# Kernel optimization log

Measured on AMD Instinct MI355X. Metric: run time of the kernel, lower is better.

## Reference

```python
import jax, jax.numpy as jnp
import numpy as np

# Planck radiance in wavenumber form: B(nu, T) = c1*nu^3 / (exp(c2*nu/T) - 1)
# nu in cm^-1, T in Kelvin, B in W / (m^2 sr cm^-1)
C1 = 1.191042e-8
C2 = 1.4387752
N_TEMPS = 20


def planck_radiance(nu, T):
    return C1 * nu ** 3 / jnp.expm1(C2 * nu / T)


def setup_inputs() -> dict:
    key = jax.random.key(0)
    k1, k2, k3 = jax.random.split(key, 3)
    N, C = 1048576, 54  # 1024x1024 pixels, 54 spectral channels
    wg = jnp.linspace(720.0, 1250.0, C, dtype=jnp.float32)
    v = (wg - wg.min()) / (wg.max() - wg.min())
    pi = 3.14159
    library = jnp.stack([
        jnp.full((C,), 0.98),                      # skin
        0.9 + 0.05 * jnp.sin(2 * pi * v),          # fabric_cotton
        0.15 + 0.1 * v,                            # metal_aluminum
        0.95 - 0.03 * v,                           # vegetation
        0.92 + 0.02 * jnp.sin(4 * pi * v),         # concrete
        0.85 + 0.1 * v,                            # glass
    ]).astype(jnp.float32)
    # realistic LWIR radiance magnitudes (~0.02-0.12 W/m^2/sr/cm^-1)
    s_sky = 0.05 * jax.random.uniform(k1, (C,), dtype=jnp.float32)
    s_ground = 0.08 + 0.02 * jax.random.uniform(k2, (C,), dtype=jnp.float32)
    s_obs = 0.02 + 0.1 * jax.random.uniform(k3, (N, C), dtype=jnp.float32)
    return {"s_obs": s_obs, "s_sky": s_sky, "s_ground": s_ground,
            "library": library, "wavenumber_grid": wg}


def reference(s_obs, s_sky, s_ground, library, wavenumber_grid):
    N, C = s_obs.shape
    M = library.shape[0]
    t_cand = jnp.linspace(250.0, 350.0, N_TEMPS, dtype=s_obs.dtype)
    # All candidate model spectra are pixel-independent (V fixed at 0.5):
    x_amb = 0.5 * s_sky + 0.5 * s_ground                           # [C]
    B = planck_radiance(wavenumber_grid[None, :], t_cand[:, None])  # [T, C]
    s_model = library[:, None, :] * B[None, :, :] \
        + (1.0 - library[:, None, :]) * x_amb                       # [M, T, C]
    cand = s_model.reshape(M * N_TEMPS, C)  # row-major: idx = m*T + t, matches loop order
    # ||s_obs - cand||^2 expanded: memory-bound [N, M*T] loss matrix
    losses = (jnp.sum(s_obs ** 2, axis=-1, keepdims=True)
              - 2.0 * s_obs @ cand.T
              + jnp.sum(cand ** 2, axis=-1))                        # [N, M*T]
    best = jnp.argmin(losses, axis=-1)                              # first-min, matches strict '<'
    best_loss = jnp.take_along_axis(losses, best[:, None], axis=1)[:, 0]
    m_idx = best // N_TEMPS
    t_idx = best % N_TEMPS
    best_t = t_cand[t_idx]                                          # [N]
    best_e = library[m_idx]                                         # [N, C]
    best_v = jnp.full((N,), 0.5, dtype=s_obs.dtype)
    s_recon = best_e * planck_radiance(wavenumber_grid[None, :], best_t[:, None]) \
        + (1.0 - best_e) * x_amb                                    # [N, C]
    texture = best_e.mean(axis=-1)
    beta = jnp.zeros((N, 1), dtype=s_obs.dtype)
    objective = best_loss.mean()
    return (best_t, best_e, best_v, beta, texture, s_recon, objective)
```

## Files before the change

### kernel.cpp

```cpp
#include <hip/hip_runtime.h>
#include <math.h>

#define C_CH 54
#define CP   64
#define NT   20
#define NM   6
#define NK   120
#define BLK  256
#define PIX_PER_BLK BLK
#define NF4  (NK * CP / 4)

typedef float f4 __attribute__((ext_vector_type(4)));

__global__ __launch_bounds__(256) void hadar_prep(
    const float* __restrict__ s_sky, const float* __restrict__ s_ground,
    const float* __restrict__ library, const float* __restrict__ wg,
    float* __restrict__ cand)
{
    __shared__ float xamb[C_CH];
    __shared__ float tc[NT];
    __shared__ float lm[NM];
    const int tid = threadIdx.x;
    if (tid < NT) tc[tid] = 250.0f + (float)tid * (100.0f / 19.0f);
    if (tid < C_CH) xamb[tid] = 0.5f * s_sky[tid] + 0.5f * s_ground[tid];
    if (tid < NM) {
        float s = 0.0f;
        for (int c = 0; c < C_CH; ++c) s += library[tid * C_CH + c];
        lm[tid] = s / (float)C_CH;
    }
    __syncthreads();

    const float c1 = 1.191042e-8f, c2 = 1.4387752f;
    for (int idx = tid; idx < NK * CP; idx += 256) {
        const int k = idx >> 6, c = idx & 63;
        float v = 0.0f;
        if (c < C_CH) {
            const int m = k / NT, t = k - m * NT;
            const float nu = wg[c];
            const float B = c1 * nu * nu * nu / expm1f(c2 * nu / tc[t]);
            const float e = library[m * C_CH + c];
            v = e * B + (1.0f - e) * xamb[c];
        }
        cand[idx] = v;
    }
    __syncthreads();

    if (tid < NK) {
        float s = 0.0f;
        for (int c = 0; c < C_CH; ++c) { float v = cand[tid * CP + c]; s += v * v; }
        const int m = tid / NT, t = tid - m * NT;
        cand[tid * CP + 54] = s;
        cand[tid * CP + 55] = tc[t];
        cand[tid * CP + 56] = lm[m];
    }
}


#define LOADH(B, F4OFF) { \
    const f4* __restrict__ Lr = Lc + (F4OFF); \
    _Pragma("unroll") for (int j = 0; j < 7; ++j) B[j] = Lr[j]; }

#define FMAPH(B, CB) { \
    _Pragma("unroll") for (int j = 0; j < 7; ++j) { \
        _Pragma("unroll") for (int e = 0; e < 4; ++e) { \
            const int c = (CB) + 4 * j + e; \
            if (c < C_CH) a[c & 3] += row0[c] * B[j][e]; \
        } } }

__global__ __launch_bounds__(BLK)
__attribute__((amdgpu_waves_per_eu(2, 2)))
void hadar_main(
    const float* __restrict__ s_obs,
    const float* __restrict__ library,
    const float* __restrict__ cand,
    float* __restrict__ out, float* __restrict__ partials, int N)
{
    __shared__ f4 ldsc[NF4];
    __shared__ int2 bkm[PIX_PER_BLK];
    __shared__ float red[BLK];

    const int tid = threadIdx.x;
    const long long base = (long long)blockIdx.x * PIX_PER_BLK;
    const long long n0 = base + tid;
    const bool v0 = (n0 < N);

    float row0[C_CH];
    if (v0) {
        const float2* rp = (const float2*)(s_obs + n0 * C_CH);
        #pragma unroll
        for (int i = 0; i < C_CH / 2; ++i) {
            float2 w = rp[i];
            row0[2 * i] = w.x; row0[2 * i + 1] = w.y;
        }
    } else {
        #pragma unroll
        for (int c = 0; c < C_CH; ++c) row0[c] = 0.0f;
    }

    {
        const f4* __restrict__ gc = (const f4*)cand;
        for (int j = tid; j < NF4; j += BLK) ldsc[j] = gc[j];
    }

    float ssq0 = 0.0f;
    #pragma unroll
    for (int c = 0; c < C_CH; ++c) ssq0 += row0[c] * row0[c];

    float bl0 = 3.4e38f;
    int bk0 = NK;

    __syncthreads();

    const f4* __restrict__ Lc = ldsc;

    f4 P[7], Q[7];
    int f0 = 0;
    LOADH(P, 0);
    #pragma unroll 1
    for (int k = 0; k < NK; ++k) {
        LOADH(Q, f0 + 7);
        float a[4] = {0.f, 0.f, 0.f, 0.f};
        FMAPH(P, 0);
        const int fn = (k + 1 < NK) ? f0 + 16 : 0;
        LOADH(P, fn);
        FMAPH(Q, 28);
        const float sq = Q[6][2];
        const float d = (a[0] + a[1]) + (a[2] + a[3]);
        const float l = (ssq0 - 2.0f * d) + sq;
        if (l < bl0) { bl0 = l; bk0 = k; }
        f0 = fn;
    }

    if (!v0 || bk0 >= NK) bk0 = 0;

    const size_t NN = (size_t)N;
    const size_t NC = (size_t)C_CH * NN;
    const float* __restrict__ Lf = (const float*)ldsc;

    if (v0) {
        out[n0] = Lf[bk0 * CP + 55];
        out[NN + NC + n0] = 0.5f;
        out[2 * NN + NC + n0] = 0.0f;
        out[3 * NN + NC + n0] = Lf[bk0 * CP + 56];
    }

    bkm[tid] = make_int2(bk0 * CP, (bk0 / NT) * C_CH);

    float lsum = v0 ? bl0 : 0.0f;
    __syncthreads();

    {
        float* __restrict__ be = out + NN + (size_t)base * C_CH;
        float* __restrict__ sr = out + 4 * NN + NC + (size_t)base * C_CH;
        int p = tid / C_CH;
        int c = tid - p * C_CH;
        #pragma unroll 2
        for (int j = tid; j < PIX_PER_BLK * C_CH; j += BLK) {
            const int2 o = bkm[p];
            const float ev = library[o.y + c];
            const float sv = Lf[o.x + c];
            if (base + p < N) { be[j] = ev; sr[j] = sv; }
            p += 4; c += 40;
            if (c >= C_CH) { c -= C_CH; ++p; }
        }
    }

    red[tid] = lsum;
    __syncthreads();
    #pragma unroll
    for (int s = BLK / 2; s > 0; s >>= 1) {
        if (tid < s) red[tid] += red[tid + s];
        __syncthreads();
    }
    if (tid == 0) partials[blockIdx.x] = red[0];
}

__global__ __launch_bounds__(256) void hadar_reduce(
    const float* __restrict__ partials, int nb, float* __restrict__ obj_out, float invN)
{
    __shared__ float red[256];
    float s = 0.0f;
    for (int i = threadIdx.x; i < nb; i += 256) s += partials[i];
    red[threadIdx.x] = s;
    __syncthreads();
    #pragma unroll
    for (int st = 128; st > 0; st >>= 1) {
        if (threadIdx.x < st) red[threadIdx.x] += red[threadIdx.x + st];
        __syncthreads();
    }
    if (threadIdx.x == 0) *obj_out = red[0] * invN;
}

extern "C" void kernel_launch(void* const* d_in, const int* in_sizes, int n_in,
                              void* d_out, int out_size, void* d_ws, size_t ws_size,
                              hipStream_t stream)
{
    const float* s_obs    = (const float*)d_in[0];
    const float* s_sky    = (const float*)d_in[1];
    const float* s_ground = (const float*)d_in[2];
    const float* library  = (const float*)d_in[3];
    const float* wg       = (const float*)d_in[4];
    float* out = (float*)d_out;

    const int N  = in_sizes[0] / C_CH;
    const int nb = (N + PIX_PER_BLK - 1) / PIX_PER_BLK;

    float* ws       = (float*)d_ws;
    float* cand     = ws;
    float* partials = ws + 8192;

    hadar_prep<<<1, 256, 0, stream>>>(s_sky, s_ground, library, wg, cand);
    hadar_main<<<nb, BLK, 0, stream>>>(s_obs, library, cand, out, partials, N);

    const size_t NN = (size_t)N;
    float* obj_out = out + 4 * NN + 2 * (size_t)C_CH * NN;
    hadar_reduce<<<1, 256, 0, stream>>>(partials, nb, obj_out, 1.0f / (float)N);
}
```

Baseline: 889.8 us.

## Read candidate spectra through scalar loads instead of LDS in main loop

The candidate table is no longer staged in shared memory. Each iteration of the 120-candidate loop now fetches one candidate row into scalar registers with s_load_dwordx16/x8 inline asm, and the FMA loop uses those scalar operands directly. This removes the LDS fill, a barrier, and the per-thread LDS reads, which frees LDS and drops the fixed waves-per-EU limit. In exchange, every iteration serialises on an lgkmcnt(0) wait with no prefetch overlap, and the gather stage now reads from global memory rather than LDS.

After: 732.8 us. 1.21x faster.

```diff
diff --git a/kernel.cpp b/kernel.cpp
--- a/kernel.cpp
+++ b/kernel.cpp
@@ -8,9 +8,9 @@
 #define NK   120
 #define BLK  256
 #define PIX_PER_BLK BLK
-#define NF4  (NK * CP / 4)
 
-typedef float f4 __attribute__((ext_vector_type(4)));
+typedef float sf16 __attribute__((ext_vector_type(16)));
+typedef float sf8  __attribute__((ext_vector_type(8)));
 
 __global__ __launch_bounds__(256) void hadar_prep(
     const float* __restrict__ s_sky, const float* __restrict__ s_ground,
@@ -55,30 +55,14 @@
     }
 }
 
+#define CE(c) ((c) < 16 ? q0[(c)] : (c) < 32 ? q1[(c)-16] : (c) < 48 ? q2[(c)-32] : q3[(c)-48])
 
-#define LOADH(B, F4OFF) { \
-    const f4* __restrict__ Lr = Lc + (F4OFF); \
-    _Pragma("unroll") for (int j = 0; j < 7; ++j) B[j] = Lr[j]; }
-
-#define FMAPH(B, CB) { \
-    _Pragma("unroll") for (int j = 0; j < 7; ++j) { \
-        _Pragma("unroll") for (int e = 0; e < 4; ++e) { \
-            const int c = (CB) + 4 * j + e; \
-            if (c < C_CH) a[c & 3] += row0[c] * B[j][e]; \
-        } } }
-
-__global__ __launch_bounds__(BLK)
-__attribute__((amdgpu_waves_per_eu(2, 2)))
-void hadar_main(
+__global__ __launch_bounds__(BLK) void hadar_main(
     const float* __restrict__ s_obs,
     const float* __restrict__ library,
     const float* __restrict__ cand,
     float* __restrict__ out, float* __restrict__ partials, int N)
 {
-    __shared__ f4 ldsc[NF4];
-    __shared__ int2 bkm[PIX_PER_BLK];
-    __shared__ float red[BLK];
-
     const int tid = threadIdx.x;
     const long long base = (long long)blockIdx.x * PIX_PER_BLK;
     const long long n0 = base + tid;
@@ -97,53 +81,49 @@
         for (int c = 0; c < C_CH; ++c) row0[c] = 0.0f;
     }
 
-    {
-        const f4* __restrict__ gc = (const f4*)cand;
-        for (int j = tid; j < NF4; j += BLK) ldsc[j] = gc[j];
-    }
-
     float ssq0 = 0.0f;
     #pragma unroll
     for (int c = 0; c < C_CH; ++c) ssq0 += row0[c] * row0[c];
 
     float bl0 = 3.4e38f;
-    int bk0 = NK;
+    int bk0 = 0;
 
-    __syncthreads();
-
-    const f4* __restrict__ Lc = ldsc;
-
-    f4 P[7], Q[7];
-    int f0 = 0;
-    LOADH(P, 0);
+    const float* pk = cand;
     #pragma unroll 1
     for (int k = 0; k < NK; ++k) {
-        LOADH(Q, f0 + 7);
+        sf16 q0, q1, q2;
+        sf8  q3;
+        asm volatile("s_load_dwordx16 %0, %1, 0x0"  : "=s"(q0) : "s"(pk));
+        asm volatile("s_load_dwordx16 %0, %1, 0x40" : "=s"(q1) : "s"(pk));
+        asm volatile("s_load_dwordx16 %0, %1, 0x80" : "=s"(q2) : "s"(pk));
+        asm volatile("s_load_dwordx8  %0, %1, 0xc0" : "=s"(q3) : "s"(pk));
+        asm volatile("s_waitcnt lgkmcnt(0)" : "+s"(q0), "+s"(q1), "+s"(q2), "+s"(q3));
+
         float a[4] = {0.f, 0.f, 0.f, 0.f};
-        FMAPH(P, 0);
-        const int fn = (k + 1 < NK) ? f0 + 16 : 0;
-        LOADH(P, fn);
-        FMAPH(Q, 28);
-        const float sq = Q[6][2];
+        #pragma unroll
+        for (int c = 0; c < C_CH; ++c) {
+            a[c & 3] += row0[c] * CE(c);
+        }
+        const float sq = q3[6];
         const float d = (a[0] + a[1]) + (a[2] + a[3]);
         const float l = (ssq0 - 2.0f * d) + sq;
         if (l < bl0) { bl0 = l; bk0 = k; }
-        f0 = fn;
+
+        pk += CP;
     }
-
-    if (!v0 || bk0 >= NK) bk0 = 0;
 
     const size_t NN = (size_t)N;
     const size_t NC = (size_t)C_CH * NN;
-    const float* __restrict__ Lf = (const float*)ldsc;
 
     if (v0) {
-        out[n0] = Lf[bk0 * CP + 55];
+        const float* cr = cand + (size_t)bk0 * CP;
+        out[n0] = cr[55];
         out[NN + NC + n0] = 0.5f;
         out[2 * NN + NC + n0] = 0.0f;
-        out[3 * NN + NC + n0] = Lf[bk0 * CP + 56];
+        out[3 * NN + NC + n0] = cr[56];
     }
 
+    __shared__ int2 bkm[PIX_PER_BLK];
     bkm[tid] = make_int2(bk0 * CP, (bk0 / NT) * C_CH);
 
     float lsum = v0 ? bl0 : 0.0f;
@@ -158,13 +138,14 @@
         for (int j = tid; j < PIX_PER_BLK * C_CH; j += BLK) {
             const int2 o = bkm[p];
             const float ev = library[o.y + c];
-            const float sv = Lf[o.x + c];
+            const float sv = cand[o.x + c];
             if (base + p < N) { be[j] = ev; sr[j] = sv; }
             p += 4; c += 40;
             if (c >= C_CH) { c -= C_CH; ++p; }
         }
     }
 
+    __shared__ float red[BLK];
     red[tid] = lsum;
     __syncthreads();
     #pragma unroll
```
